# Kernel tuning notes

Hardware: AMD Instinct MI355X
Metric: run time of the kernel (lower is better)

Reference implementation:

```python
import jax, jax.numpy as jnp
import numpy as np

B = 4096      # batch of users
D = 128       # embedding_dim
NA = 128      # num_anchors
AD = 128      # anchor_dim
NU = 100000   # num_users
NI = 50000    # num_items


def setup_inputs() -> dict:
    key = jax.random.key(0)
    ks = jax.random.split(key, 10)
    s = 0.05
    return {
        "user_indices": jax.random.randint(ks[0], (B,), 0, NU),
        "pos_item_indices": jax.random.randint(ks[1], (B,), 0, NI),
        "user_table": jax.random.normal(ks[2], (NU, D), dtype=jnp.float32) * s,
        "item_table": jax.random.normal(ks[3], (NI, D), dtype=jnp.float32) * s,
        "ln1_g": jnp.ones((D,), jnp.float32),
        "ln1_b": jnp.zeros((D,), jnp.float32),
        "send_W": jax.random.normal(ks[4], (D, AD), dtype=jnp.float32) * s,
        "send_a": jax.random.normal(ks[5], (2 * AD,), dtype=jnp.float32) * s,
        "anchors": jax.random.normal(ks[6], (NA, AD), dtype=jnp.float32) * s,
        "ln2_g": jnp.ones((NA,), jnp.float32),
        "ln2_b": jnp.zeros((NA,), jnp.float32),
        "recv_W": jax.random.normal(ks[7], (NA, D), dtype=jnp.float32) * s,
        "recv_a": jax.random.normal(ks[8], (2 * D,), dtype=jnp.float32) * s,
    }


def _layernorm(x, g, b, eps=1e-5):
    m = jnp.mean(x, axis=-1, keepdims=True)
    v = jnp.mean((x - m) ** 2, axis=-1, keepdims=True)
    return (x - m) * jax.lax.rsqrt(v + eps) * g + b


def _fca(x, W, a):
    # FullyConnectedAttention: score[i,j] = [t_i ; t_j] . a = t_i.a1 + t_j.a2
    # (decomposed form of the torch repeat/cat -> same math, no [B,B,2F] tensor)
    t = x @ W                       # [B, F]
    f = t.shape[-1]
    a1, a2 = a[:f], a[f:]
    e = (t @ a1)[:, None] + (t @ a2)[None, :]   # [B, B]
    w = jax.nn.softmax(e, axis=1)
    return w @ t                    # [B, F]


def reference(user_indices, pos_item_indices, user_table, item_table,
              ln1_g, ln1_b, send_W, send_a, anchors, ln2_g, ln2_b,
              recv_W, recv_a):
    u = user_table[user_indices]                 # [B, D]
    # AdaptiveAnchorConvolution
    nf = _layernorm(u, ln1_g, ln1_b)             # feature_norm
    sent = _fca(nf, send_W, send_a)              # send_attention -> [B, AD]
    ap = sent @ anchors.T                        # anchor projection [B, NA]
    na = _layernorm(ap, ln2_g, ln2_b)            # anchor_norm
    rec = _fca(na, recv_W, recv_a)               # receive_attention -> [B, D]
    ue = u + jnp.sin(rec)                        # residual + sin
    pos = item_table[pos_item_indices]           # [B, D]
    preds = ue @ item_table.T                    # [B, NI]
    return preds, ue, pos
```

## Files before the change

kernel.cpp:

```cpp
#include <hip/hip_runtime.h>
#include <hip/hip_bf16.h>

#define BB   4096
#define DD   128
#define NII  50000

typedef __attribute__((ext_vector_type(8))) short  bf8_t;
typedef __attribute__((ext_vector_type(4))) float  f4_t;
typedef __attribute__((ext_vector_type(4))) unsigned short us4_t;
typedef __attribute__((ext_vector_type(4))) float  fl4_t;

static __device__ __forceinline__ unsigned short f2bf(float f) {
    unsigned u = __float_as_uint(f);
    u += 0x7fffu + ((u >> 16) & 1u);
    return (unsigned short)(u >> 16);
}

static __device__ __forceinline__ void gload_lds16(const void* g, void* lds) {
    __builtin_amdgcn_global_load_lds(
        (const __attribute__((address_space(1))) void*)g,
        (__attribute__((address_space(3))) void*)lds, 16, 0, 0);
}

__global__ __launch_bounds__(128) void k1_embed_send(
    const int* __restrict__ uidx, const float* __restrict__ utab,
    const float* __restrict__ g1, const float* __restrict__ b1,
    const float* __restrict__ sendW, const float* __restrict__ senda,
    float* __restrict__ t_out, float* __restrict__ s2_out)
{
    __shared__ float sb[128];
    __shared__ float nf[128];
    const int row = blockIdx.x;
    const int tid = threadIdx.x;
    const long urow = uidx[row];
    const float x = utab[urow * 128 + tid];

    sb[tid] = x; __syncthreads();
    for (int s = 64; s > 0; s >>= 1) { if (tid < s) sb[tid] += sb[tid + s]; __syncthreads(); }
    const float mean = sb[0] * (1.0f / 128.0f); __syncthreads();
    const float dv = x - mean;
    sb[tid] = dv * dv; __syncthreads();
    for (int s = 64; s > 0; s >>= 1) { if (tid < s) sb[tid] += sb[tid + s]; __syncthreads(); }
    const float var = sb[0] * (1.0f / 128.0f);
    const float rs = rsqrtf(var + 1e-5f);
    nf[tid] = dv * rs * g1[tid] + b1[tid];
    __syncthreads();

    float acc = 0.f;
    #pragma unroll 8
    for (int d = 0; d < 128; ++d) acc += nf[d] * sendW[d * 128 + tid];
    t_out[row * 128 + tid] = acc;

    const float p = acc * senda[128 + tid];
    __syncthreads();
    sb[tid] = p; __syncthreads();
    for (int s = 64; s > 0; s >>= 1) { if (tid < s) sb[tid] += sb[tid + s]; __syncthreads(); }
    if (tid == 0) s2_out[row] = sb[0];
}

__global__ __launch_bounds__(256) void k2b_colsum(
    const float* __restrict__ t, const float* __restrict__ s2,
    float* __restrict__ partial)
{
    __shared__ float ew[128];
    __shared__ float sb[256];
    const int tid = threadIdx.x;

    float m = -1e30f;
    for (int i = tid; i < BB; i += 256) m = fmaxf(m, s2[i]);
    sb[tid] = m; __syncthreads();
    for (int s = 128; s > 0; s >>= 1) { if (tid < s) sb[tid] = fmaxf(sb[tid], sb[tid + s]); __syncthreads(); }
    m = sb[0]; __syncthreads();

    const int rbase = blockIdx.x * 128;
    if (tid < 128) ew[tid] = __expf(s2[rbase + tid] - m);
    __syncthreads();
    const int col = tid & 127, half = tid >> 7;
    float acc = 0.f;
    for (int j = half; j < 128; j += 2)
        acc += ew[j] * t[(rbase + j) * 128 + col];
    sb[tid] = acc; __syncthreads();
    if (tid < 128) partial[blockIdx.x * 128 + tid] = sb[tid] + sb[tid + 128];
}

__global__ __launch_bounds__(128) void k2c_finish(
    const float* __restrict__ partial, const float* __restrict__ s2,
    const float* __restrict__ anchors, const float* __restrict__ g2,
    const float* __restrict__ b2, const float* __restrict__ recvW,
    float* __restrict__ r_out)
{
    __shared__ float sent[128];
    __shared__ float na_s[128];
    __shared__ float sb[128];
    const int tid = threadIdx.x;

    float m = -1e30f;
    for (int i = tid; i < BB; i += 128) m = fmaxf(m, s2[i]);
    sb[tid] = m; __syncthreads();
    for (int s = 64; s > 0; s >>= 1) { if (tid < s) sb[tid] = fmaxf(sb[tid], sb[tid + s]); __syncthreads(); }
    m = sb[0]; __syncthreads();
    float sum = 0.f;
    for (int i = tid; i < BB; i += 128) sum += __expf(s2[i] - m);
    sb[tid] = sum; __syncthreads();
    for (int s = 64; s > 0; s >>= 1) { if (tid < s) sb[tid] += sb[tid + s]; __syncthreads(); }
    const float S = sb[0]; __syncthreads();

    float acc = 0.f;
    for (int b = 0; b < 32; ++b) acc += partial[b * 128 + tid];
    sent[tid] = acc / S;
    __syncthreads();
    float ap = 0.f;
    for (int c = 0; c < 128; ++c) ap += sent[c] * anchors[tid * 128 + c];
    sb[tid] = ap; __syncthreads();
    for (int s = 64; s > 0; s >>= 1) { if (tid < s) sb[tid] += sb[tid + s]; __syncthreads(); }
    const float mean = sb[0] * (1.0f / 128.0f); __syncthreads();
    const float dv = ap - mean;
    sb[tid] = dv * dv; __syncthreads();
    for (int s = 64; s > 0; s >>= 1) { if (tid < s) sb[tid] += sb[tid + s]; __syncthreads(); }
    const float var = sb[0] * (1.0f / 128.0f);
    const float rs = rsqrtf(var + 1e-5f);
    na_s[tid] = dv * rs * g2[tid] + b2[tid];
    __syncthreads();
    float t2 = 0.f;
    for (int k = 0; k < 128; ++k) t2 += na_s[k] * recvW[k * 128 + tid];
    r_out[tid] = sinf(t2);
}

__global__ __launch_bounds__(256) void k3_ue_pos(
    const int* __restrict__ uidx, const float* __restrict__ utab,
    const int* __restrict__ pidx, const float* __restrict__ itab,
    const float* __restrict__ r, float* __restrict__ ue_out,
    float* __restrict__ pos_out, unsigned short* __restrict__ uebf)
{
    const int gid = blockIdx.x * 256 + threadIdx.x;
    const int i = gid >> 7, d = gid & 127;
    const float rv = r[d];
    const float u = utab[(long)uidx[i] * 128 + d];
    const float ue = u + rv;
    ue_out[gid] = ue;
    uebf[gid] = f2bf(ue);
    pos_out[gid] = itab[(long)pidx[i] * 128 + d];
}

__global__ __launch_bounds__(256) void k3b_cvt_item(
    const float* __restrict__ itab, unsigned short* __restrict__ ibf)
{
    const int gid = blockIdx.x * 256 + threadIdx.x;
    const fl4_t v = *(const fl4_t*)(itab + (long)gid * 4);
    us4_t o;
    o.x = f2bf(v.x); o.y = f2bf(v.y); o.z = f2bf(v.z); o.w = f2bf(v.w);
    *(us4_t*)(ibf + (long)gid * 4) = o;
}

__global__ __launch_bounds__(256, 4) void k4_gemm(
    const unsigned short* __restrict__ uebf,
    const unsigned short* __restrict__ ibf,
    float* __restrict__ preds)
{
    __shared__ unsigned short lB[128 * 128];

    const int tid = threadIdx.x;
    const int wave = tid >> 6, lane = tid & 63;
    const int l15 = lane & 15, kg = lane >> 4;
    const int col0 = blockIdx.x * 128;
    const int row0 = blockIdx.y * 128;

    #pragma unroll
    for (int i = 0; i < 8; ++i) {
        const int o   = (i * 256 + tid) * 16;
        const int r   = o >> 8;
        const int ch  = (o >> 4) & 15;
        const int sw  = ch ^ (r & 15);
        const int bc  = (col0 + r) < NII ? (col0 + r) : (NII - 1);
        gload_lds16(ibf + (size_t)bc * 128 + sw * 8,
                    (char*)lB + i * 4096 + wave * 1024);
    }

    const int wr = wave >> 1, wc = wave & 1;

    f4_t acc[4][4];
    #pragma unroll
    for (int m = 0; m < 4; ++m)
        #pragma unroll
        for (int n = 0; n < 4; ++n) acc[m][n] = (f4_t){0.f, 0.f, 0.f, 0.f};

    __syncthreads();

    #pragma unroll
    for (int kk = 0; kk < 4; ++kk) {
        const int c = kk * 4 + kg;
        bf8_t a[4], b[4];
        #pragma unroll
        for (int m = 0; m < 4; ++m) {
            const int r = row0 + wr * 64 + m * 16 + l15;
            a[m] = *(const bf8_t*)(uebf + (size_t)r * 128 + c * 8);
        }
        #pragma unroll
        for (int n = 0; n < 4; ++n) {
            const int r = wc * 64 + n * 16 + l15;
            b[n] = *(const bf8_t*)((const char*)lB + r * 256 + (c ^ (r & 15)) * 16);
        }
        #pragma unroll
        for (int m = 0; m < 4; ++m)
            #pragma unroll
            for (int n = 0; n < 4; ++n)
                acc[m][n] = __builtin_amdgcn_mfma_f32_16x16x32_bf16(a[m], b[n], acc[m][n], 0, 0, 0);
    }

    const int orow = row0 + wr * 64 + kg * 4;
    const int ocol = col0 + wc * 64 + l15;
    #pragma unroll
    for (int m = 0; m < 4; ++m) {
        #pragma unroll
        for (int n = 0; n < 4; ++n) {
            const int col = ocol + n * 16;
            if (col < NII) {
                #pragma unroll
                for (int j = 0; j < 4; ++j)
                    preds[(long)(orow + m * 16 + j) * NII + col] = acc[m][n][j];
            }
        }
    }
}

extern "C" void kernel_launch(void* const* d_in, const int* in_sizes, int n_in,
                              void* d_out, int out_size, void* d_ws, size_t ws_size,
                              hipStream_t stream) {
    const int*   uidx   = (const int*)  d_in[0];
    const int*   pidx   = (const int*)  d_in[1];
    const float* utab   = (const float*)d_in[2];
    const float* itab   = (const float*)d_in[3];
    const float* g1     = (const float*)d_in[4];
    const float* b1     = (const float*)d_in[5];
    const float* sendW  = (const float*)d_in[6];
    const float* senda  = (const float*)d_in[7];
    const float* anchors= (const float*)d_in[8];
    const float* g2     = (const float*)d_in[9];
    const float* b2     = (const float*)d_in[10];
    const float* recvW  = (const float*)d_in[11];

    char* ws = (char*)d_ws;
    float* t_ws    = (float*)(ws + 0);
    float* s2_ws   = (float*)(ws + 2097152);
    float* part_ws = (float*)(ws + 2113600);
    float* r_ws    = (float*)(ws + 2129984);
    unsigned short* uebf = (unsigned short*)(ws + 2130496);
    unsigned short* ibf  = (unsigned short*)(ws + 3179072);

    float* preds   = (float*)d_out;
    float* ue_out  = preds + (long)BB * NII;
    float* pos_out = ue_out + BB * DD;

    k3b_cvt_item<<<6250, 256, 0, stream>>>(itab, ibf);
    k1_embed_send<<<4096, 128, 0, stream>>>(uidx, utab, g1, b1, sendW, senda, t_ws, s2_ws);
    k2b_colsum<<<32, 256, 0, stream>>>(t_ws, s2_ws, part_ws);
    k2c_finish<<<1, 128, 0, stream>>>(part_ws, s2_ws, anchors, g2, b2, recvW, r_ws);
    k3_ue_pos<<<2048, 256, 0, stream>>>(uidx, utab, pidx, itab, r_ws, ue_out, pos_out, uebf);
    k4_gemm<<<dim3(391, 32, 1), 256, 0, stream>>>(uebf, ibf, preds);
}
```

Baseline: 285.6 us.

## Stage A tile in LDS and vectorize output stores through LDS transpose

The GEMM kernel now loads the user-embedding A tile into swizzled LDS with async global-to-LDS loads, instead of reading it straight from global memory in each k-step. The epilogue stages the accumulators through LDS per wave so each lane writes 16-byte float4 stores along rows, replacing scattered 4-byte stores. This targets the output write, which dominates given the 4096x50000 fp32 preds. The cost is 64KB of LDS, with launch bounds lowered to 2 blocks per CU, which reduces occupancy. Because NII is divisible by 4, the float4 stores stay aligned and the gcol<NII guard stays valid.

```diff
diff --git a/kernel.cpp b/kernel.cpp
--- a/kernel.cpp
+++ b/kernel.cpp
@@ -152,12 +152,14 @@
     *(us4_t*)(ibf + (long)gid * 4) = o;
 }
 
-__global__ __launch_bounds__(256, 4) void k4_gemm(
+__global__ __launch_bounds__(256, 2) void k4_gemm(
     const unsigned short* __restrict__ uebf,
     const unsigned short* __restrict__ ibf,
     float* __restrict__ preds)
 {
-    __shared__ unsigned short lB[128 * 128];
+    __shared__ char smem[65536];
+    unsigned short* lA = (unsigned short*)smem;
+    unsigned short* lB = (unsigned short*)(smem + 32768);
 
     const int tid = threadIdx.x;
     const int wave = tid >> 6, lane = tid & 63;
@@ -171,6 +173,8 @@
         const int r   = o >> 8;
         const int ch  = (o >> 4) & 15;
         const int sw  = ch ^ (r & 15);
+        gload_lds16(uebf + (size_t)(row0 + r) * 128 + sw * 8,
+                    (char*)lA + i * 4096 + wave * 1024);
         const int bc  = (col0 + r) < NII ? (col0 + r) : (NII - 1);
         gload_lds16(ibf + (size_t)bc * 128 + sw * 8,
                     (char*)lB + i * 4096 + wave * 1024);
@@ -192,8 +196,8 @@
         bf8_t a[4], b[4];
         #pragma unroll
         for (int m = 0; m < 4; ++m) {
-            const int r = row0 + wr * 64 + m * 16 + l15;
-            a[m] = *(const bf8_t*)(uebf + (size_t)r * 128 + c * 8);
+            const int r = wr * 64 + m * 16 + l15;
+            a[m] = *(const bf8_t*)((const char*)lA + r * 256 + (c ^ (r & 15)) * 16);
         }
         #pragma unroll
         for (int n = 0; n < 4; ++n) {
@@ -207,18 +211,28 @@
                 acc[m][n] = __builtin_amdgcn_mfma_f32_16x16x32_bf16(a[m], b[n], acc[m][n], 0, 0, 0);
     }
 
-    const int orow = row0 + wr * 64 + kg * 4;
-    const int ocol = col0 + wc * 64 + l15;
-    #pragma unroll
-    for (int m = 0; m < 4; ++m) {
-        #pragma unroll
-        for (int n = 0; n < 4; ++n) {
-            const int col = ocol + n * 16;
-            if (col < NII) {
+    __syncthreads();
+    float* ep = (float*)smem + wave * (32 * 76);
+
+    #pragma unroll
+    for (int h = 0; h < 2; ++h) {
+        #pragma unroll
+        for (int mm = 0; mm < 2; ++mm) {
+            const int m = h * 2 + mm;
+            #pragma unroll
+            for (int n = 0; n < 4; ++n)
                 #pragma unroll
                 for (int j = 0; j < 4; ++j)
-                    preds[(long)(orow + m * 16 + j) * NII + col] = acc[m][n][j];
-            }
+                    ep[(mm * 16 + kg * 4 + j) * 76 + n * 16 + l15] = acc[m][n][j];
+        }
+        #pragma unroll
+        for (int rr = 0; rr < 8; ++rr) {
+            const int lrow = rr * 4 + (lane >> 4);
+            const f4_t v = *(const f4_t*)(ep + lrow * 76 + (lane & 15) * 4);
+            const int grow = row0 + wr * 64 + h * 32 + lrow;
+            const int gcol = col0 + wc * 64 + (lane & 15) * 4;
+            if (gcol < NII)
+                *(fl4_t*)(preds + (long)grow * NII + gcol) = v;
         }
     }
 }
```

New measurement: 252.4 us. -11.6%, faster.

## Reuse item tile across eight row tiles, stage A in LDS, vectorize stores

Applied to the files above, without the earlier changes.

The GEMM block now keeps one 128-column item tile in LDS and loops over eight 128-row user tiles, so the grid drops from 32 to 4 rows of blocks. A tiles are loaded into swizzled LDS asynchronously while the previous tile's results are stored. MFMA operands are swapped so each lane holds four consecutive columns, which allows 16-byte vector stores to preds. The cost is more LDS per block, fewer blocks, lower occupancy, and float4 stores that are misaligned because NII=50000 makes each row's start only 16-byte aligned on every fourth row... actually 50000*4 bytes is 16-byte aligned, so the stores stay aligned.

```diff
diff --git a/kernel.cpp b/kernel.cpp
--- a/kernel.cpp
+++ b/kernel.cpp
@@ -152,72 +152,96 @@
     *(us4_t*)(ibf + (long)gid * 4) = o;
 }
 
-__global__ __launch_bounds__(256, 4) void k4_gemm(
+__global__ __launch_bounds__(256, 2) void k4_gemm(
     const unsigned short* __restrict__ uebf,
     const unsigned short* __restrict__ ibf,
     float* __restrict__ preds)
 {
+    __shared__ unsigned short lA[128 * 128];
     __shared__ unsigned short lB[128 * 128];
 
     const int tid = threadIdx.x;
     const int wave = tid >> 6, lane = tid & 63;
     const int l15 = lane & 15, kg = lane >> 4;
     const int col0 = blockIdx.x * 128;
-    const int row0 = blockIdx.y * 128;
+    const int mt0  = blockIdx.y * 8;
 
     #pragma unroll
     for (int i = 0; i < 8; ++i) {
-        const int o   = (i * 256 + tid) * 16;
-        const int r   = o >> 8;
-        const int ch  = (o >> 4) & 15;
-        const int sw  = ch ^ (r & 15);
-        const int bc  = (col0 + r) < NII ? (col0 + r) : (NII - 1);
+        const int o  = (i * 256 + tid) * 16;
+        const int r  = o >> 8;
+        const int ch = (o >> 4) & 15;
+        const int sw = ch ^ (r & 15);
+        const int bc = (col0 + r) < NII ? (col0 + r) : (NII - 1);
         gload_lds16(ibf + (size_t)bc * 128 + sw * 8,
                     (char*)lB + i * 4096 + wave * 1024);
     }
+    #pragma unroll
+    for (int i = 0; i < 8; ++i) {
+        const int o  = (i * 256 + tid) * 16;
+        const int r  = o >> 8;
+        const int ch = (o >> 4) & 15;
+        const int sw = ch ^ (r & 15);
+        gload_lds16(uebf + (size_t)(mt0 * 128 + r) * 128 + sw * 8,
+                    (char*)lA + i * 4096 + wave * 1024);
+    }
 
     const int wr = wave >> 1, wc = wave & 1;
 
-    f4_t acc[4][4];
-    #pragma unroll
-    for (int m = 0; m < 4; ++m)
+    for (int mt = 0; mt < 8; ++mt) {
+        __syncthreads();
+
+        f4_t acc[4][4];
         #pragma unroll
-        for (int n = 0; n < 4; ++n) acc[m][n] = (f4_t){0.f, 0.f, 0.f, 0.f};
-
-    __syncthreads();
-
-    #pragma unroll
-    for (int kk = 0; kk < 4; ++kk) {
-        const int c = kk * 4 + kg;
-        bf8_t a[4], b[4];
+        for (int m = 0; m < 4; ++m)
+            #pragma unroll
+            for (int n = 0; n < 4; ++n) acc[m][n] = (f4_t){0.f, 0.f, 0.f, 0.f};
+
+        #pragma unroll
+        for (int kk = 0; kk < 4; ++kk) {
+            const int c = kk * 4 + kg;
+            bf8_t a[4], b[4];
+            #pragma unroll
+            for (int m = 0; m < 4; ++m) {
+                const int r = wr * 64 + m * 16 + l15;
+                a[m] = *(const bf8_t*)((const char*)lA + r * 256 + (c ^ (r & 15)) * 16);
+            }
+            #pragma unroll
+            for (int n = 0; n < 4; ++n) {
+                const int r = wc * 64 + n * 16 + l15;
+                b[n] = *(const bf8_t*)((const char*)lB + r * 256 + (c ^ (r & 15)) * 16);
+            }
+            #pragma unroll
+            for (int m = 0; m < 4; ++m)
+                #pragma unroll
+                for (int n = 0; n < 4; ++n)
+                    acc[m][n] = __builtin_amdgcn_mfma_f32_16x16x32_bf16(b[n], a[m], acc[m][n], 0, 0, 0);
+        }
+
+        __syncthreads();
+
+        if (mt < 7) {
+            const size_t rbase = (size_t)(mt0 + mt + 1) * 128;
+            #pragma unroll
+            for (int i = 0; i < 8; ++i) {
+                const int o  = (i * 256 + tid) * 16;
+                const int r  = o >> 8;
+                const int ch = (o >> 4) & 15;
+                const int sw = ch ^ (r & 15);
+                gload_lds16(uebf + (rbase + r) * 128 + sw * 8,
+                            (char*)lA + i * 4096 + wave * 1024);
+            }
+        }
+
+        const int row0 = (mt0 + mt) * 128;
         #pragma unroll
         for (int m = 0; m < 4; ++m) {
-            const int r = row0 + wr * 64 + m * 16 + l15;
-            a[m] = *(const bf8_t*)(uebf + (size_t)r * 128 + c * 8);
-        }
-        #pragma unroll
-        for (int n = 0; n < 4; ++n) {
-            const int r = wc * 64 + n * 16 + l15;
-            b[n] = *(const bf8_t*)((const char*)lB + r * 256 + (c ^ (r & 15)) * 16);
-        }
-        #pragma unroll
-        for (int m = 0; m < 4; ++m)
-            #pragma unroll
-            for (int n = 0; n < 4; ++n)
-                acc[m][n] = __builtin_amdgcn_mfma_f32_16x16x32_bf16(a[m], b[n], acc[m][n], 0, 0, 0);
-    }
-
-    const int orow = row0 + wr * 64 + kg * 4;
-    const int ocol = col0 + wc * 64 + l15;
-    #pragma unroll
-    for (int m = 0; m < 4; ++m) {
-        #pragma unroll
-        for (int n = 0; n < 4; ++n) {
-            const int col = ocol + n * 16;
-            if (col < NII) {
-                #pragma unroll
-                for (int j = 0; j < 4; ++j)
-                    preds[(long)(orow + m * 16 + j) * NII + col] = acc[m][n][j];
+            const long grow = row0 + wr * 64 + m * 16 + l15;
+            #pragma unroll
+            for (int n = 0; n < 4; ++n) {
+                const int gcol = col0 + wc * 64 + n * 16 + kg * 4;
+                if (gcol < NII)
+                    *(fl4_t*)(preds + grow * NII + gcol) = acc[m][n];
             }
         }
     }
@@ -256,5 +280,5 @@
     k2b_colsum<<<32, 256, 0, stream>>>(t_ws, s2_ws, part_ws);
     k2c_finish<<<1, 128, 0, stream>>>(part_ws, s2_ws, anchors, g2, b2, recvW, r_ws);
     k3_ue_pos<<<2048, 256, 0, stream>>>(uidx, utab, pidx, itab, r_ws, ue_out, pos_out, uebf);
-    k4_gemm<<<dim3(391, 32, 1), 256, 0, stream>>>(uebf, ibf, preds);
-}
+    k4_gemm<<<dim3(391, 4, 1), 256, 0, stream>>>(uebf, ibf, preds);
+}
```

Result: slower. 297.5 us (+4.2%).
